# Kernel optimization log

Measured on AMD Instinct MI355X. Metric: run time of the kernel, lower is better.

The kernel has to match this reference:

```python
import jax, jax.numpy as jnp
import numpy as np
from jax import lax

C = 32    # feats_channels
CT = 16   # transform_channels
B, D, H, W = 1, 16, 16, 32  # N = D*H*W = 8192


def _bcast(v):
    return v[None, :, None, None, None]


def conv1(x, w):
    # 1x1x1 Conv3d, no bias: w [O, I], x [b, I, d, h, w]
    return jnp.einsum('oi,bidhw->bodhw', w, x)


def cbr(x, w, s, b):
    # Conv1x1x1 + inference BatchNorm (folded to scale s / bias b) + ReLU
    return jax.nn.relu(conv1(x, w) * _bcast(s) + _bcast(b))


def setup_inputs() -> dict:
    key = jax.random.key(0)
    ks = jax.random.split(key, 16)

    def wmat(k, shape, scale=0.05):
        return jax.random.normal(k, shape, jnp.float32) * scale

    def bn(k, n):
        k1, k2 = jax.random.split(k)
        s = 1.0 + 0.05 * jax.random.normal(k1, (n,), jnp.float32)
        b = 0.05 * jax.random.normal(k2, (n,), jnp.float32)
        return s, b

    inp = {'x': jax.random.normal(ks[0], (B, C, D, H, W), jnp.float32)}
    # query_project: 2 convs (C->CT, CT->CT), each conv+BN+ReLU
    inp['wq1'] = wmat(ks[1], (CT, C));  inp['sq1'], inp['bq1'] = bn(ks[2], CT)
    inp['wq2'] = wmat(ks[3], (CT, CT)); inp['sq2'], inp['bq2'] = bn(ks[4], CT)
    # key_project: 2 convs (2C->CT, CT->CT)
    inp['wk1'] = wmat(ks[5], (CT, 2 * C)); inp['sk1'], inp['bk1'] = bn(ks[6], CT)
    inp['wk2'] = wmat(ks[7], (CT, CT));    inp['sk2'], inp['bk2'] = bn(ks[8], CT)
    # value_project: 1 conv (2C->CT) + BN + ReLU
    inp['wv'] = wmat(ks[9], (CT, 2 * C)); inp['sv'], inp['bv'] = bn(ks[10], CT)
    # out_project: 1 conv (CT->C) + BN + ReLU
    inp['wo'] = wmat(ks[11], (C, CT)); inp['so'], inp['bo'] = bn(ks[12], C)
    # bottleneck: Conv3d(2C->C, k=3, pad=1, no bias) + BN + LeakyReLU(0.1)
    inp['wbot'] = wmat(ks[13], (C, 2 * C, 3, 3, 3), 0.02)
    inp['sbot'], inp['bbot'] = bn(ks[14], C)
    return inp


def reference(x, wq1, sq1, bq1, wq2, sq2, bq2,
              wk1, sk1, bk1, wk2, sk2, bk2,
              wv, sv, bv, wo, so, bo, wbot, sbot, bbot):
    b, c, d, h, w = x.shape
    # AdaptiveAvgPool2d((1,1)) on (b, c*d, h, w) = mean over (h, w) per (c,d);
    # bilinear upsample from 1x1 is a constant broadcast.
    xg = jnp.mean(x, axis=(3, 4), keepdims=True)
    key_feats = jnp.concatenate([jnp.broadcast_to(xg, x.shape), x], axis=1)  # [b, 2c, d, h, w]

    q = cbr(cbr(x, wq1, sq1, bq1), wq2, sq2, bq2)          # [b, CT, d, h, w]
    k = cbr(cbr(key_feats, wk1, sk1, bk1), wk2, sk2, bk2)  # [b, CT, d, h, w]
    v = cbr(key_feats, wv, sv, bv)                          # [b, CT, d, h, w]

    n = d * h * w
    q = q.reshape(b, CT, n).transpose(0, 2, 1)  # [b, N, CT]
    k = k.reshape(b, CT, n)                     # [b, CT, N]
    v = v.reshape(b, CT, n).transpose(0, 2, 1)  # [b, N, CT]

    sim = jnp.einsum('bnc,bcm->bnm', q, k) * (CT ** -0.5)   # [b, N, N]
    sim = jax.nn.softmax(sim, axis=-1)
    ctx = jnp.einsum('bnm,bmc->bnc', sim, v)                # [b, N, CT]
    ctx = ctx.transpose(0, 2, 1).reshape(b, CT, d, h, w)
    ctx = cbr(ctx, wo, so, bo)                              # [b, C, d, h, w]

    fused = jnp.concatenate([x, ctx], axis=1)               # [b, 2C, d, h, w]
    y = lax.conv_general_dilated(
        fused, wbot, window_strides=(1, 1, 1), padding='SAME',
        dimension_numbers=('NCDHW', 'OIDHW', 'NCDHW'))
    y = y * _bcast(sbot) + _bcast(bbot)
    return jnp.where(y > 0, y, 0.1 * y)  # LeakyReLU(0.1)
```

## Files before the change

### kernel.cpp

```cpp
#include <hip/hip_runtime.h>

typedef unsigned int u32;
typedef unsigned short u16;
typedef float f32x16 __attribute__((ext_vector_type(16)));
typedef __bf16 bf16x8 __attribute__((ext_vector_type(8)));
union BF8 { u32 w[4]; bf16x8 v; };

#define DEVI static __device__ __forceinline__
DEVI u32 pk_bf16(float lo, float hi) {
  u32 r;
  asm("v_cvt_pk_bf16_f32 %0, %1, %2" : "=v"(r) : "v"(lo), "v"(hi));
  return r;
}
DEVI u16 bf1(float x) { return (u16)(pk_bf16(x, 0.0f) & 0xffffu); }

#define WB_WREP  0
#define WB_QS    131072
#define WB_K     393216
#define WB_VTS   655360
#define WB_FUS   917504

__global__ __launch_bounds__(512) void k_prep(
    const float* __restrict__ x,
    const float* __restrict__ wq1, const float* __restrict__ sq1, const float* __restrict__ bq1,
    const float* __restrict__ wq2, const float* __restrict__ sq2, const float* __restrict__ bq2,
    const float* __restrict__ wk1, const float* __restrict__ sk1, const float* __restrict__ bk1,
    const float* __restrict__ wk2, const float* __restrict__ sk2, const float* __restrict__ bk2,
    const float* __restrict__ wv,  const float* __restrict__ sv,  const float* __restrict__ bv,
    const float* __restrict__ wbot, const float* __restrict__ sbot,
    u16* __restrict__ qs, u16* __restrict__ kbm, u16* __restrict__ vts,
    u16* __restrict__ fus, u16* __restrict__ wrep) {
  const int tid = threadIdx.x;
  const int bid = blockIdx.x;
  if (bid >= 256) {
    const int rb = bid - 256;
#pragma unroll
    for (int e = 0; e < 8; ++e) {
      const int idx = rb * 4096 + tid * 8 + e;
      if (idx < 55296) {
        const int tap = idx >> 11, rem = idx & 2047, o = rem >> 6, i = rem & 63;
        wrep[idx] = bf1(wbot[(o * 64 + i) * 27 + tap] * sbot[o]);
      }
    }
    return;
  }
  __shared__ float SH[1664];
  const int n0 = bid << 5;
  const int d = n0 >> 9;
  {
    const int c = tid >> 4, part = tid & 15;
    const float4* xp = (const float4*)(x + (c << 13) + (d << 9));
    float s = 0.f;
#pragma unroll
    for (int i = 0; i < 8; ++i) {
      const float4 v4 = xp[part + (i << 4)];
      s += v4.x + v4.y + v4.z + v4.w;
    }
    SH[1088 + (c << 4) + part] = s;
  }
  __syncthreads();
  if (tid < 32) {
    float s = 0.f;
#pragma unroll
    for (int j = 0; j < 16; ++j) s += SH[1088 + (tid << 4) + j];
    SH[1600 + tid] = s * (1.0f / 512.0f);
  }
  __syncthreads();
  const int nl = tid & 31, g = tid >> 5;
  const int n = n0 + nl;
  {
    float xr[32], xgv[32];
#pragma unroll
    for (int c = 0; c < 32; ++c) xr[c] = x[(c << 13) + n];
#pragma unroll
    for (int c = 0; c < 32; ++c) xgv[c] = SH[1600 + c];

    const float4* wq1f = (const float4*)wq1;
    const float4* wk1f = (const float4*)wk1;
    const float4* wvf  = (const float4*)wv;
    float dq = 0.f, dk = 0.f, dv = 0.f;
#pragma unroll
    for (int c4 = 0; c4 < 8; ++c4) {
      const float4 wa = wq1f[g * 8 + c4];
      dq += wa.x * xr[4*c4+0] + wa.y * xr[4*c4+1] + wa.z * xr[4*c4+2] + wa.w * xr[4*c4+3];
    }
#pragma unroll
    for (int c4 = 0; c4 < 8; ++c4) {
      const float4 ka = wk1f[g * 16 + c4];
      dk += ka.x * xgv[4*c4+0] + ka.y * xgv[4*c4+1] + ka.z * xgv[4*c4+2] + ka.w * xgv[4*c4+3];
      const float4 va = wvf[g * 16 + c4];
      dv += va.x * xgv[4*c4+0] + va.y * xgv[4*c4+1] + va.z * xgv[4*c4+2] + va.w * xgv[4*c4+3];
    }
#pragma unroll
    for (int c4 = 0; c4 < 8; ++c4) {
      const float4 ka = wk1f[g * 16 + 8 + c4];
      dk += ka.x * xr[4*c4+0] + ka.y * xr[4*c4+1] + ka.z * xr[4*c4+2] + ka.w * xr[4*c4+3];
      const float4 va = wvf[g * 16 + 8 + c4];
      dv += va.x * xr[4*c4+0] + va.y * xr[4*c4+1] + va.z * xr[4*c4+2] + va.w * xr[4*c4+3];
    }
    const float hq = fmaxf(dq * sq1[g] + bq1[g], 0.f);
    const float hk = fmaxf(dk * sk1[g] + bk1[g], 0.f);
    const float hv = fmaxf(dv * sv[g] + bv[g], 0.f);
    SH[nl * 17 + g] = hq;
    SH[544 + nl * 17 + g] = hk;
    vts[(bid << 9) + (g << 5) + nl] = bf1(hv);
    const int c0 = g << 1;
    *(u32*)(fus + (n << 6) + c0) = pk_bf16(xr[c0], xr[c0 + 1]);
  }
  __syncthreads();
  if (tid < 256) {
    const int nl2 = tid & 31, g2 = tid >> 5;
    const int n2 = n0 + nl2;
    const int r0 = 2 * g2, r1 = r0 + 1;
    float eq0 = 0.f, eq1 = 0.f, ek0 = 0.f, ek1 = 0.f;
#pragma unroll
    for (int j = 0; j < 16; ++j) {
      const float hq = SH[nl2 * 17 + j], hk = SH[544 + nl2 * 17 + j];
      eq0 += wq2[r0 * 16 + j] * hq;
      eq1 += wq2[r1 * 16 + j] * hq;
      ek0 += wk2[r0 * 16 + j] * hk;
      ek1 += wk2[r1 * 16 + j] * hk;
    }
    const float SC = 0.36067376022224085f;
    const float q0 = fmaxf(eq0 * (sq2[r0] * SC) + bq2[r0] * SC, 0.f);
    const float q1 = fmaxf(eq1 * (sq2[r1] * SC) + bq2[r1] * SC, 0.f);
    const float k0 = fmaxf(ek0 * sk2[r0] + bk2[r0], 0.f);
    const float k1 = fmaxf(ek1 * sk2[r1] + bk2[r1], 0.f);
    *(u32*)(qs  + (n2 << 4) + r0) = pk_bf16(q0, q1);
    *(u32*)(kbm + (n2 << 4) + r0) = pk_bf16(k0, k1);
  }
}

__global__ __launch_bounds__(1024) void k_attn(
    const u16* __restrict__ qs, const u16* __restrict__ kbm, const u16* __restrict__ vts,
    const float* __restrict__ wo, const float* __restrict__ so, const float* __restrict__ bo,
    u16* __restrict__ fus) {
  __shared__ float R[16][32][17];
  const int tid = threadIdx.x;
  const int w = tid >> 6, lane = tid & 63;
  const int l31 = lane & 31, h = lane >> 5;
  const int qb = blockIdx.x;

  const bf16x8 qf = *(const bf16x8*)(qs + (((qb << 5) + l31) << 4) + (h << 3));
  f32x16 acc_a, acc_b, z;
#pragma unroll
  for (int i = 0; i < 16; ++i) { acc_a[i] = 0.f; acc_b[i] = 0.f; z[i] = 0.f; }

  const u32 fill = (l31 == 16) ? 0x3F803F80u : 0u;
  const int kb0 = w << 9;
  const int t0 = w << 4;
  const bool vlane = (l31 < 16);
  const u16* vbase = vts + (l31 << 5) + (h << 3);

  bf16x8 kf_c = *(const bf16x8*)(kbm + ((kb0 + l31) << 4) + (h << 3));
  BF8 V1c, V2c;
#pragma unroll
  for (int j2 = 0; j2 < 4; ++j2) { V1c.w[j2] = fill; V2c.w[j2] = fill; }
  if (vlane) {
    V1c.v = *(const bf16x8*)(vbase + (t0 << 9));
    V2c.v = *(const bf16x8*)(vbase + (t0 << 9) + 16);
  }

#pragma unroll
  for (int t = 0; t < 16; ++t) {
    const bf16x8 kf = kf_c;
    const BF8 V1 = V1c, V2 = V2c;
    if (t < 15) {
      const int kbn = kb0 + ((t + 1) << 5);
      kf_c = *(const bf16x8*)(kbm + ((kbn + l31) << 4) + (h << 3));
      if (vlane) {
        const u16* vp = vbase + ((t0 + t + 1) << 9);
        V1c.v = *(const bf16x8*)vp;
        V2c.v = *(const bf16x8*)(vp + 16);
      }
    }
    const f32x16 st = __builtin_amdgcn_mfma_f32_32x32x16_bf16(kf, qf, z, 0, 0, 0);
    float pe[16];
#pragma unroll
    for (int r = 0; r < 16; ++r) pe[r] = __builtin_amdgcn_exp2f(st[r]);
    u32 a0 = pk_bf16(pe[0],  pe[1]),  a1 = pk_bf16(pe[2],  pe[3]);
    u32 a2 = pk_bf16(pe[4],  pe[5]),  a3 = pk_bf16(pe[6],  pe[7]);
    u32 b0 = pk_bf16(pe[8],  pe[9]),  b1 = pk_bf16(pe[10], pe[11]);
    u32 b2 = pk_bf16(pe[12], pe[13]), b3 = pk_bf16(pe[14], pe[15]);
    asm("v_permlane32_swap_b32 %0, %1" : "+v"(a0), "+v"(a2));
    asm("v_permlane32_swap_b32 %0, %1" : "+v"(a1), "+v"(a3));
    asm("v_permlane32_swap_b32 %0, %1" : "+v"(b0), "+v"(b2));
    asm("v_permlane32_swap_b32 %0, %1" : "+v"(b1), "+v"(b3));
    BF8 A1, A2;
    A1.w[0] = a0; A1.w[1] = a1; A1.w[2] = a2; A1.w[3] = a3;
    A2.w[0] = b0; A2.w[1] = b1; A2.w[2] = b2; A2.w[3] = b3;
    __builtin_amdgcn_s_setprio(1);
    acc_a = __builtin_amdgcn_mfma_f32_32x32x16_bf16(A1.v, V1.v, acc_a, 0, 0, 0);
    acc_b = __builtin_amdgcn_mfma_f32_32x32x16_bf16(A2.v, V2.v, acc_b, 0, 0, 0);
    __builtin_amdgcn_s_setprio(0);
  }
  if (l31 < 17) {
#pragma unroll
    for (int r = 0; r < 16; ++r) {
      const int row = (r & 3) + ((r >> 2) << 3) + (h << 2);
      R[w][row][l31] = acc_a[r] + acc_b[r];
    }
  }
  __syncthreads();
  float* Rf = &R[0][0][0];
  if (tid < 544) {
    float s0 = 0.f;
#pragma unroll
    for (int w2 = 0; w2 < 16; ++w2) s0 += Rf[w2 * 544 + tid];
    Rf[tid] = s0;
  }
  __syncthreads();
  if (tid < 512) {
    const int row = tid >> 4;
    const int o0 = (tid & 15) << 1, o1 = o0 + 1;
    const float inv = 1.0f / Rf[row * 17 + 16];
    float d0 = 0.f, d1 = 0.f;
#pragma unroll
    for (int c = 0; c < 16; ++c) {
      const float cv = Rf[row * 17 + c];
      d0 += wo[o0 * 16 + c] * cv;
      d1 += wo[o1 * 16 + c] * cv;
    }
    const float y0 = fmaxf(bo[o0] + so[o0] * d0 * inv, 0.f);
    const float y1 = fmaxf(bo[o1] + so[o1] * d1 * inv, 0.f);
    *(u32*)(fus + (((qb << 5) + row) << 6) + 32 + o0) = pk_bf16(y0, y1);
  }
}

__global__ __launch_bounds__(512) void k_conv(
    const u16* __restrict__ fus, const u16* __restrict__ wrep,
    const float* __restrict__ bbot, float* __restrict__ out) {
  __shared__ float R8[8][1024];
  const int tid = threadIdx.x;
  const int wv = tid >> 6, lane = tid & 63;
  const int l31 = lane & 31, h = lane >> 5;
  const int n0 = blockIdx.x << 5;
  const int dz = n0 >> 9, hy = (n0 >> 5) & 15;
  f32x16 acc0, acc1;
#pragma unroll
  for (int i = 0; i < 16; ++i) { acc0[i] = 0.f; acc1[i] = 0.f; }
  const int ulo = (wv * 54) >> 3, uhi = ((wv + 1) * 54) >> 3;

  const u16* bp_c; const u16* wp_c; bool ok_c;
  {
    const int tap = ulo >> 1, ch = (ulo & 1) << 1;
    const int dd = tap / 9 - 1, dh = (tap / 3) % 3 - 1, dw = tap % 3 - 1;
    ok_c = ((unsigned)(dz + dd) < 16u) & ((unsigned)(hy + dh) < 16u) &
           ((unsigned)(l31 + dw) < 32u);
    const int nn = n0 + dd * 512 + dh * 32 + dw + l31;
    bp_c = fus + (nn << 6) + (ch << 4) + (h << 3);
    wp_c = wrep + ((tap * 32 + l31) << 6) + (ch << 4) + (h << 3);
  }
  BF8 B0c, B1c;
  B0c.w[0] = B0c.w[1] = B0c.w[2] = B0c.w[3] = 0u;
  B1c.w[0] = B1c.w[1] = B1c.w[2] = B1c.w[3] = 0u;
  if (ok_c) { B0c.v = *(const bf16x8*)bp_c; B1c.v = *(const bf16x8*)(bp_c + 16); }

  for (int u = ulo; u < uhi; ++u) {
    const BF8 B0 = B0c, B1 = B1c;
    const u16* wp = wp_c;
    if (u + 1 < uhi) {
      const int un = u + 1;
      const int tap = un >> 1, ch = (un & 1) << 1;
      const int dd = tap / 9 - 1, dh = (tap / 3) % 3 - 1, dw = tap % 3 - 1;
      const bool ok = ((unsigned)(dz + dd) < 16u) & ((unsigned)(hy + dh) < 16u) &
                      ((unsigned)(l31 + dw) < 32u);
      const int nn = n0 + dd * 512 + dh * 32 + dw + l31;
      const u16* bp = fus + (nn << 6) + (ch << 4) + (h << 3);
      wp_c = wrep + ((tap * 32 + l31) << 6) + (ch << 4) + (h << 3);
      B0c.w[0] = B0c.w[1] = B0c.w[2] = B0c.w[3] = 0u;
      B1c.w[0] = B1c.w[1] = B1c.w[2] = B1c.w[3] = 0u;
      if (ok) { B0c.v = *(const bf16x8*)bp; B1c.v = *(const bf16x8*)(bp + 16); }
    }
    const bf16x8 af0 = *(const bf16x8*)wp;
    const bf16x8 af1 = *(const bf16x8*)(wp + 16);
    __builtin_amdgcn_s_setprio(1);
    acc0 = __builtin_amdgcn_mfma_f32_32x32x16_bf16(af0, B0.v, acc0, 0, 0, 0);
    acc1 = __builtin_amdgcn_mfma_f32_32x32x16_bf16(af1, B1.v, acc1, 0, 0, 0);
    __builtin_amdgcn_s_setprio(0);
  }
#pragma unroll
  for (int r = 0; r < 16; ++r) {
    const int row = (r & 3) + ((r >> 2) << 3) + (h << 2);
    R8[wv][(row << 5) + l31] = acc0[r] + acc1[r];
  }
  __syncthreads();
#pragma unroll
  for (int k2 = 0; k2 < 2; ++k2) {
    const int e = tid + (k2 << 9);
    const int row = e >> 5;
    float yv = bbot[row];
#pragma unroll
    for (int w2 = 0; w2 < 8; ++w2) yv += R8[w2][e];
    out[(row << 13) + n0 + (e & 31)] = yv > 0.f ? yv : 0.1f * yv;
  }
}

extern "C" void kernel_launch(void* const* d_in, const int* in_sizes, int n_in,
                              void* d_out, int out_size, void* d_ws, size_t ws_size,
                              hipStream_t stream) {
  const float* x    = (const float*)d_in[0];
  const float* wq1  = (const float*)d_in[1];
  const float* sq1  = (const float*)d_in[2];
  const float* bq1  = (const float*)d_in[3];
  const float* wq2  = (const float*)d_in[4];
  const float* sq2  = (const float*)d_in[5];
  const float* bq2  = (const float*)d_in[6];
  const float* wk1  = (const float*)d_in[7];
  const float* sk1  = (const float*)d_in[8];
  const float* bk1  = (const float*)d_in[9];
  const float* wk2  = (const float*)d_in[10];
  const float* sk2  = (const float*)d_in[11];
  const float* bk2  = (const float*)d_in[12];
  const float* wv   = (const float*)d_in[13];
  const float* sv   = (const float*)d_in[14];
  const float* bv   = (const float*)d_in[15];
  const float* wo   = (const float*)d_in[16];
  const float* so   = (const float*)d_in[17];
  const float* bo   = (const float*)d_in[18];
  const float* wbot = (const float*)d_in[19];
  const float* sbot = (const float*)d_in[20];
  const float* bbot = (const float*)d_in[21];
  (void)in_sizes; (void)n_in; (void)out_size; (void)ws_size;

  char* wsb = (char*)d_ws;
  u16* wrep = (u16*)(wsb + WB_WREP);
  u16* qs   = (u16*)(wsb + WB_QS);
  u16* kbm  = (u16*)(wsb + WB_K);
  u16* vts  = (u16*)(wsb + WB_VTS);
  u16* fus  = (u16*)(wsb + WB_FUS);
  float* out = (float*)d_out;

  k_prep<<<270, 512, 0, stream>>>(x, wq1, sq1, bq1, wq2, sq2, bq2,
                                  wk1, sk1, bk1, wk2, sk2, bk2,
                                  wv, sv, bv, wbot, sbot,
                                  qs, kbm, vts, fus, wrep);
  k_attn<<<256, 1024, 0, stream>>>(qs, kbm, vts, wo, so, bo, fus);
  k_conv<<<256, 512, 0, stream>>>(fus, wrep, bbot, out);
}
```

Baseline: 35.58 us.

## Split prep into smaller blocks and software-pipeline QK MFMA in attention

The prep kernel now runs 539 blocks of 256 threads, each covering 16 positions instead of 32. Each block stages its x tile in shared memory, and the xg contributions of the key and value projections are computed once per block instead of once per thread. The attention loop now issues the next QK^T MFMA one iteration ahead and splits the exp and PV MFMA into two halves, so the matrix unit can overlap with the exp work. The cost is more registers for the extra score accumulator and a doubled block count in prep.

```diff
diff --git a/kernel.cpp b/kernel.cpp
--- a/kernel.cpp
+++ b/kernel.cpp
@@ -20,7 +20,15 @@
 #define WB_VTS   655360
 #define WB_FUS   917504
 
-__global__ __launch_bounds__(512) void k_prep(
+#define SX_XT   0
+#define SX_H0   640
+#define SX_H1   912
+#define SX_P8   1184
+#define SX_XG   1440
+#define SX_DKX  1472
+#define SX_DVX  1488
+
+__global__ __launch_bounds__(256) void k_prep(
     const float* __restrict__ x,
     const float* __restrict__ wq1, const float* __restrict__ sq1, const float* __restrict__ bq1,
     const float* __restrict__ wq2, const float* __restrict__ sq2, const float* __restrict__ bq2,
@@ -32,102 +40,106 @@
     u16* __restrict__ fus, u16* __restrict__ wrep) {
   const int tid = threadIdx.x;
   const int bid = blockIdx.x;
-  if (bid >= 256) {
-    const int rb = bid - 256;
+  if (bid >= 512) {
+    const int rb = bid - 512;
 #pragma unroll
     for (int e = 0; e < 8; ++e) {
-      const int idx = rb * 4096 + tid * 8 + e;
-      if (idx < 55296) {
-        const int tap = idx >> 11, rem = idx & 2047, o = rem >> 6, i = rem & 63;
-        wrep[idx] = bf1(wbot[(o * 64 + i) * 27 + tap] * sbot[o]);
-      }
+      const int idx = rb * 2048 + tid * 8 + e;
+      const int tap = idx >> 11, rem = idx & 2047, o = rem >> 6, i = rem & 63;
+      wrep[idx] = bf1(wbot[(o * 64 + i) * 27 + tap] * sbot[o]);
     }
     return;
   }
-  __shared__ float SH[1664];
-  const int n0 = bid << 5;
-  const int d = n0 >> 9;
+  __shared__ float SH[1504];
+  const int n0 = bid << 4;
+  const int d = bid >> 5;
   {
-    const int c = tid >> 4, part = tid & 15;
+    const int c = tid >> 3, part = tid & 7;
     const float4* xp = (const float4*)(x + (c << 13) + (d << 9));
     float s = 0.f;
 #pragma unroll
-    for (int i = 0; i < 8; ++i) {
-      const float4 v4 = xp[part + (i << 4)];
+    for (int i = 0; i < 16; ++i) {
+      const float4 v4 = xp[part + (i << 3)];
       s += v4.x + v4.y + v4.z + v4.w;
     }
-    SH[1088 + (c << 4) + part] = s;
+    SH[SX_P8 + (c << 3) + part] = s;
+    if (tid < 128) {
+      const int cc = tid >> 2, ii = tid & 3;
+      const float4 v4 = *(const float4*)(x + (cc << 13) + n0 + (ii << 2));
+      *(float4*)(&SH[SX_XT + cc * 20 + (ii << 2)]) = v4;
+    }
   }
   __syncthreads();
   if (tid < 32) {
     float s = 0.f;
 #pragma unroll
-    for (int j = 0; j < 16; ++j) s += SH[1088 + (tid << 4) + j];
-    SH[1600 + tid] = s * (1.0f / 512.0f);
-  }
-  __syncthreads();
-  const int nl = tid & 31, g = tid >> 5;
+    for (int j = 0; j < 8; ++j) s += SH[SX_P8 + (tid << 3) + j];
+    SH[SX_XG + tid] = s * (1.0f / 512.0f);
+    const float4* wxf = (tid < 16) ? (const float4*)wk1 : (const float4*)wv;
+    const int g = tid & 15;
+    float dx = 0.f;
+#pragma unroll
+    for (int c4 = 0; c4 < 8; ++c4) {
+      const float4 wa = wxf[g * 16 + c4];
+      dx += wa.x * SH[SX_XG + 4*c4] + wa.y * SH[SX_XG + 4*c4+1] +
+            wa.z * SH[SX_XG + 4*c4+2] + wa.w * SH[SX_XG + 4*c4+3];
+    }
+    SH[(tid < 16 ? SX_DKX : SX_DVX - 16) + tid] = dx;
+  }
+  __syncthreads();
+  const int nl = tid & 15, g = tid >> 4;
   const int n = n0 + nl;
   {
-    float xr[32], xgv[32];
-#pragma unroll
-    for (int c = 0; c < 32; ++c) xr[c] = x[(c << 13) + n];
-#pragma unroll
-    for (int c = 0; c < 32; ++c) xgv[c] = SH[1600 + c];
-
+    float xc[32];
+#pragma unroll
+    for (int c = 0; c < 32; ++c) xc[c] = SH[SX_XT + c * 20 + nl];
     const float4* wq1f = (const float4*)wq1;
     const float4* wk1f = (const float4*)wk1;
     const float4* wvf  = (const float4*)wv;
-    float dq = 0.f, dk = 0.f, dv = 0.f;
+    float dq = 0.f, dk = SH[SX_DKX + g], dv = SH[SX_DVX + g];
 #pragma unroll
     for (int c4 = 0; c4 < 8; ++c4) {
       const float4 wa = wq1f[g * 8 + c4];
-      dq += wa.x * xr[4*c4+0] + wa.y * xr[4*c4+1] + wa.z * xr[4*c4+2] + wa.w * xr[4*c4+3];
-    }
-#pragma unroll
-    for (int c4 = 0; c4 < 8; ++c4) {
-      const float4 ka = wk1f[g * 16 + c4];
-      dk += ka.x * xgv[4*c4+0] + ka.y * xgv[4*c4+1] + ka.z * xgv[4*c4+2] + ka.w * xgv[4*c4+3];
-      const float4 va = wvf[g * 16 + c4];
-      dv += va.x * xgv[4*c4+0] + va.y * xgv[4*c4+1] + va.z * xgv[4*c4+2] + va.w * xgv[4*c4+3];
-    }
-#pragma unroll
-    for (int c4 = 0; c4 < 8; ++c4) {
+      dq += wa.x * xc[4*c4+0] + wa.y * xc[4*c4+1] + wa.z * xc[4*c4+2] + wa.w * xc[4*c4+3];
       const float4 ka = wk1f[g * 16 + 8 + c4];
-      dk += ka.x * xr[4*c4+0] + ka.y * xr[4*c4+1] + ka.z * xr[4*c4+2] + ka.w * xr[4*c4+3];
+      dk += ka.x * xc[4*c4+0] + ka.y * xc[4*c4+1] + ka.z * xc[4*c4+2] + ka.w * xc[4*c4+3];
       const float4 va = wvf[g * 16 + 8 + c4];
-      dv += va.x * xr[4*c4+0] + va.y * xr[4*c4+1] + va.z * xr[4*c4+2] + va.w * xr[4*c4+3];
+      dv += va.x * xc[4*c4+0] + va.y * xc[4*c4+1] + va.z * xc[4*c4+2] + va.w * xc[4*c4+3];
     }
     const float hq = fmaxf(dq * sq1[g] + bq1[g], 0.f);
     const float hk = fmaxf(dk * sk1[g] + bk1[g], 0.f);
     const float hv = fmaxf(dv * sv[g] + bv[g], 0.f);
-    SH[nl * 17 + g] = hq;
-    SH[544 + nl * 17 + g] = hk;
-    vts[(bid << 9) + (g << 5) + nl] = bf1(hv);
+    SH[SX_H0 + nl * 17 + g] = hq;
+    SH[SX_H1 + nl * 17 + g] = hk;
+    vts[((n >> 5) << 9) + (g << 5) + (n & 31)] = bf1(hv);
     const int c0 = g << 1;
-    *(u32*)(fus + (n << 6) + c0) = pk_bf16(xr[c0], xr[c0 + 1]);
-  }
-  __syncthreads();
-  if (tid < 256) {
-    const int nl2 = tid & 31, g2 = tid >> 5;
-    const int n2 = n0 + nl2;
-    const int r0 = 2 * g2, r1 = r0 + 1;
-    float eq0 = 0.f, eq1 = 0.f, ek0 = 0.f, ek1 = 0.f;
+    *(u32*)(fus + (n << 6) + c0) = pk_bf16(SH[SX_XT + c0 * 20 + nl],
+                                           SH[SX_XT + (c0 + 1) * 20 + nl]);
+  }
+  __syncthreads();
+  {
+    const int op = tid >> 4;
+    const bool isq = (op < 8);
+    const int r0 = (op & 7) << 1, r1 = r0 + 1;
+    const float* w2 = isq ? wq2 : wk2;
+    const float* Hrow = &SH[(isq ? SX_H0 : SX_H1) + nl * 17];
+    float e0 = 0.f, e1 = 0.f;
 #pragma unroll
     for (int j = 0; j < 16; ++j) {
-      const float hq = SH[nl2 * 17 + j], hk = SH[544 + nl2 * 17 + j];
-      eq0 += wq2[r0 * 16 + j] * hq;
-      eq1 += wq2[r1 * 16 + j] * hq;
-      ek0 += wk2[r0 * 16 + j] * hk;
-      ek1 += wk2[r1 * 16 + j] * hk;
-    }
-    const float SC = 0.36067376022224085f;
-    const float q0 = fmaxf(eq0 * (sq2[r0] * SC) + bq2[r0] * SC, 0.f);
-    const float q1 = fmaxf(eq1 * (sq2[r1] * SC) + bq2[r1] * SC, 0.f);
-    const float k0 = fmaxf(ek0 * sk2[r0] + bk2[r0], 0.f);
-    const float k1 = fmaxf(ek1 * sk2[r1] + bk2[r1], 0.f);
-    *(u32*)(qs  + (n2 << 4) + r0) = pk_bf16(q0, q1);
-    *(u32*)(kbm + (n2 << 4) + r0) = pk_bf16(k0, k1);
+      const float hv2 = Hrow[j];
+      e0 += w2[r0 * 16 + j] * hv2;
+      e1 += w2[r1 * 16 + j] * hv2;
+    }
+    if (isq) {
+      const float SC = 0.36067376022224085f;
+      const float q0 = fmaxf(e0 * (sq2[r0] * SC) + bq2[r0] * SC, 0.f);
+      const float q1 = fmaxf(e1 * (sq2[r1] * SC) + bq2[r1] * SC, 0.f);
+      *(u32*)(qs + (n << 4) + r0) = pk_bf16(q0, q1);
+    } else {
+      const float k0 = fmaxf(e0 * sk2[r0] + bk2[r0], 0.f);
+      const float k1 = fmaxf(e1 * sk2[r1] + bk2[r1], 0.f);
+      *(u32*)(kbm + (n << 4) + r0) = pk_bf16(k0, k1);
+    }
   }
 }
 
@@ -151,8 +163,9 @@
   const int t0 = w << 4;
   const bool vlane = (l31 < 16);
   const u16* vbase = vts + (l31 << 5) + (h << 3);
-
-  bf16x8 kf_c = *(const bf16x8*)(kbm + ((kb0 + l31) << 4) + (h << 3));
+  const u16* krow = kbm + (l31 << 4) + (h << 3);
+
+  bf16x8 kf_c = *(const bf16x8*)(krow + (kb0 << 4));
   BF8 V1c, V2c;
 #pragma unroll
   for (int j2 = 0; j2 < 4; ++j2) { V1c.w[j2] = fill; V2c.w[j2] = fill; }
@@ -160,39 +173,44 @@
     V1c.v = *(const bf16x8*)(vbase + (t0 << 9));
     V2c.v = *(const bf16x8*)(vbase + (t0 << 9) + 16);
   }
+  f32x16 st = __builtin_amdgcn_mfma_f32_32x32x16_bf16(kf_c, qf, z, 0, 0, 0);
+  kf_c = *(const bf16x8*)(krow + ((kb0 + 32) << 4));
 
 #pragma unroll
   for (int t = 0; t < 16; ++t) {
-    const bf16x8 kf = kf_c;
+    f32x16 st_next;
+    if (t < 15) st_next = __builtin_amdgcn_mfma_f32_32x32x16_bf16(kf_c, qf, z, 0, 0, 0);
     const BF8 V1 = V1c, V2 = V2c;
-    if (t < 15) {
-      const int kbn = kb0 + ((t + 1) << 5);
-      kf_c = *(const bf16x8*)(kbm + ((kbn + l31) << 4) + (h << 3));
-      if (vlane) {
-        const u16* vp = vbase + ((t0 + t + 1) << 9);
-        V1c.v = *(const bf16x8*)vp;
-        V2c.v = *(const bf16x8*)(vp + 16);
-      }
-    }
-    const f32x16 st = __builtin_amdgcn_mfma_f32_32x32x16_bf16(kf, qf, z, 0, 0, 0);
+    if (t < 14) kf_c = *(const bf16x8*)(krow + ((kb0 + ((t + 2) << 5)) << 4));
+    if (t < 15 && vlane) {
+      const u16* vp = vbase + ((t0 + t + 1) << 9);
+      V1c.v = *(const bf16x8*)vp;
+      V2c.v = *(const bf16x8*)(vp + 16);
+    }
     float pe[16];
 #pragma unroll
-    for (int r = 0; r < 16; ++r) pe[r] = __builtin_amdgcn_exp2f(st[r]);
-    u32 a0 = pk_bf16(pe[0],  pe[1]),  a1 = pk_bf16(pe[2],  pe[3]);
-    u32 a2 = pk_bf16(pe[4],  pe[5]),  a3 = pk_bf16(pe[6],  pe[7]);
+    for (int r = 0; r < 8; ++r) pe[r] = __builtin_amdgcn_exp2f(st[r]);
+    u32 a0 = pk_bf16(pe[0], pe[1]), a1 = pk_bf16(pe[2], pe[3]);
+    u32 a2 = pk_bf16(pe[4], pe[5]), a3 = pk_bf16(pe[6], pe[7]);
+    asm("v_permlane32_swap_b32 %0, %1" : "+v"(a0), "+v"(a2));
+    asm("v_permlane32_swap_b32 %0, %1" : "+v"(a1), "+v"(a3));
+    BF8 A1;
+    A1.w[0] = a0; A1.w[1] = a1; A1.w[2] = a2; A1.w[3] = a3;
+    __builtin_amdgcn_s_setprio(1);
+    acc_a = __builtin_amdgcn_mfma_f32_32x32x16_bf16(A1.v, V1.v, acc_a, 0, 0, 0);
+    __builtin_amdgcn_s_setprio(0);
+#pragma unroll
+    for (int r = 8; r < 16; ++r) pe[r] = __builtin_amdgcn_exp2f(st[r]);
     u32 b0 = pk_bf16(pe[8],  pe[9]),  b1 = pk_bf16(pe[10], pe[11]);
     u32 b2 = pk_bf16(pe[12], pe[13]), b3 = pk_bf16(pe[14], pe[15]);
-    asm("v_permlane32_swap_b32 %0, %1" : "+v"(a0), "+v"(a2));
-    asm("v_permlane32_swap_b32 %0, %1" : "+v"(a1), "+v"(a3));
     asm("v_permlane32_swap_b32 %0, %1" : "+v"(b0), "+v"(b2));
     asm("v_permlane32_swap_b32 %0, %1" : "+v"(b1), "+v"(b3));
-    BF8 A1, A2;
-    A1.w[0] = a0; A1.w[1] = a1; A1.w[2] = a2; A1.w[3] = a3;
+    BF8 A2;
     A2.w[0] = b0; A2.w[1] = b1; A2.w[2] = b2; A2.w[3] = b3;
     __builtin_amdgcn_s_setprio(1);
-    acc_a = __builtin_amdgcn_mfma_f32_32x32x16_bf16(A1.v, V1.v, acc_a, 0, 0, 0);
     acc_b = __builtin_amdgcn_mfma_f32_32x32x16_bf16(A2.v, V2.v, acc_b, 0, 0, 0);
     __builtin_amdgcn_s_setprio(0);
+    if (t < 15) st = st_next;
   }
   if (l31 < 17) {
 #pragma unroll
@@ -331,7 +349,7 @@
   u16* fus  = (u16*)(wsb + WB_FUS);
   float* out = (float*)d_out;
 
-  k_prep<<<270, 512, 0, stream>>>(x, wq1, sq1, bq1, wq2, sq2, bq2,
+  k_prep<<<539, 256, 0, stream>>>(x, wq1, sq1, bq1, wq2, sq2, bq2,
                                   wk1, sk1, bk1, wk2, sk2, bk2,
                                   wv, sv, bv, wbot, sbot,
                                   qs, kbm, vts, fus, wrep);
```

Result: faster. 33.45 us (-6.0%).
